# Performance work log

Measured on AMD Instinct MI355X. Metric: run time of the kernel, lower is better.

## Reference

```python
import jax, jax.numpy as jnp
import numpy as np
from jax import lax

LOOKBACK = 336
N_FEATURES = 164
HORIZON = 96
D_MODEL = 64
D_STATE = 16
D_CONV = 4
EXPAND = 2
D_INNER = EXPAND * D_MODEL  # 128
DT_RANK = (D_MODEL + 15) // 16  # 4
MLP_HIDDEN = 64
BATCH = 512


def setup_inputs() -> dict:
    key = jax.random.key(0)
    ks = jax.random.split(key, 20)
    f32 = jnp.float32
    inp = {}
    inp["x_raw"] = jax.random.normal(ks[0], (BATCH, LOOKBACK), f32)
    inp["x_features"] = jax.random.normal(ks[1], (BATCH, N_FEATURES), f32)
    # embed Linear(1, d_model)
    inp["embed_W"] = jax.random.normal(ks[2], (1, D_MODEL), f32) * 0.5
    inp["embed_b"] = jnp.zeros((D_MODEL,), f32)
    # Mamba params (mamba-ssm layout, stored as [in, out] for matmul)
    inp["in_W"] = jax.random.normal(ks[3], (D_MODEL, 2 * D_INNER), f32) * (1.0 / np.sqrt(D_MODEL))
    inp["conv_W"] = jax.random.normal(ks[4], (D_INNER, D_CONV), f32) * 0.3
    inp["conv_b"] = jnp.zeros((D_INNER,), f32)
    inp["xproj_W"] = jax.random.normal(ks[5], (D_INNER, DT_RANK + 2 * D_STATE), f32) * (1.0 / np.sqrt(D_INNER))
    inp["dt_W"] = jax.random.normal(ks[6], (DT_RANK, D_INNER), f32) * (1.0 / np.sqrt(DT_RANK))
    inp["dt_b"] = jax.random.uniform(ks[7], (D_INNER,), f32, -4.0, -2.0)  # softplus -> small dt
    # A_log init = log(arange(1..d_state)) broadcast over d_inner, as in mamba-ssm
    inp["A_log"] = jnp.log(jnp.broadcast_to(jnp.arange(1, D_STATE + 1, dtype=f32), (D_INNER, D_STATE)))
    inp["D"] = jnp.ones((D_INNER,), f32)
    inp["out_W"] = jax.random.normal(ks[8], (D_INNER, D_MODEL), f32) * (1.0 / np.sqrt(D_INNER))
    # MLP stream
    inp["mlp_W1"] = jax.random.normal(ks[9], (N_FEATURES, MLP_HIDDEN), f32) * (1.0 / np.sqrt(N_FEATURES))
    inp["mlp_b1"] = jnp.zeros((MLP_HIDDEN,), f32)
    inp["mlp_W2"] = jax.random.normal(ks[10], (MLP_HIDDEN, MLP_HIDDEN // 2), f32) * (1.0 / np.sqrt(MLP_HIDDEN))
    inp["mlp_b2"] = jnp.zeros((MLP_HIDDEN // 2,), f32)
    # prediction head
    fin = D_MODEL + MLP_HIDDEN // 2
    inp["head_W"] = jax.random.normal(ks[11], (fin, HORIZON), f32) * (1.0 / np.sqrt(fin))
    inp["head_b"] = jnp.zeros((HORIZON,), f32)
    return inp


def silu(x):
    return x * jax.nn.sigmoid(x)


def mamba_block(u, in_W, conv_W, conv_b, xproj_W, dt_W, dt_b, A_log, D, out_W):
    # u: [B, L, d_model]
    B_, L, _ = u.shape
    xz = u @ in_W                      # [B, L, 2*D_INNER]
    x, z = jnp.split(xz, 2, axis=-1)   # each [B, L, D_INNER]
    # causal depthwise conv1d (pad left d_conv-1), then SiLU
    xc = x.transpose(0, 2, 1)          # [B, D_INNER, L]
    kern = conv_W[:, None, :]          # [D_INNER, 1, K] (OIH)
    xc = lax.conv_general_dilated(xc, kern, window_strides=(1,),
                                  padding=[(D_CONV - 1, 0)],
                                  dimension_numbers=("NCH", "OIH", "NCH"),
                                  feature_group_count=D_INNER)
    xc = silu(xc + conv_b[None, :, None])
    x = xc.transpose(0, 2, 1)          # [B, L, D_INNER]
    # input-dependent SSM params
    x_dbl = x @ xproj_W                # [B, L, DT_RANK + 2*D_STATE]
    dt = x_dbl[..., :DT_RANK]
    Bm = x_dbl[..., DT_RANK:DT_RANK + D_STATE]          # [B, L, N]
    Cm = x_dbl[..., DT_RANK + D_STATE:]                 # [B, L, N]
    delta = jax.nn.softplus(dt @ dt_W + dt_b)           # [B, L, D_INNER]
    A = -jnp.exp(A_log)                                 # [D_INNER, N]

    # selective scan over time
    def step(h, inps):
        d_t, B_t, C_t, x_t = inps  # [B,Di], [B,N], [B,N], [B,Di]
        dA = jnp.exp(d_t[:, :, None] * A[None])              # [B, Di, N]
        dBx = (d_t * x_t)[:, :, None] * B_t[:, None, :]      # [B, Di, N]
        h = dA * h + dBx
        y_t = jnp.einsum("bdn,bn->bd", h, C_t)
        return h, y_t

    h0 = jnp.zeros((B_, D_INNER, D_STATE), u.dtype)
    seq = (delta.transpose(1, 0, 2), Bm.transpose(1, 0, 2),
           Cm.transpose(1, 0, 2), x.transpose(1, 0, 2))
    _, ys = lax.scan(step, h0, seq)        # ys: [L, B, D_INNER]
    y = ys.transpose(1, 0, 2) + x * D[None, None, :]
    y = y * silu(z)
    return y @ out_W                        # [B, L, d_model]


def reference(x_raw, x_features, embed_W, embed_b, in_W, conv_W, conv_b,
              xproj_W, dt_W, dt_b, A_log, D, out_W,
              mlp_W1, mlp_b1, mlp_W2, mlp_b2, head_W, head_b):
    # embed raw series: [B, L] -> [B, L, 1] -> [B, L, d_model]
    h = x_raw[..., None] @ embed_W + embed_b
    h = mamba_block(h, in_W, conv_W, conv_b, xproj_W, dt_W, dt_b, A_log, D, out_W)
    h_mamba_out = h[:, -1, :]                       # [B, d_model]
    h_mlp = jax.nn.relu(x_features @ mlp_W1 + mlp_b1) @ mlp_W2 + mlp_b2
    h_final = jnp.concatenate([h_mamba_out, h_mlp], axis=1)
    return h_final @ head_W + head_b                # [B, horizon]
```

## Files before the change

### kernel.cpp

```cpp
#include <hip/hip_runtime.h>
#include <math.h>

#define LOOKBACK 336
#define NFEAT    164
#define HORIZON  96
#define DMODEL   64
#define DSTATE   16
#define DINNER   128
#define MLPH     64
#define BATCH    512
#define XCP      132
#define NG       4
#define GSEG     84
#define CHK      12
#define NCH      7
#define HSTR     20

typedef float v2f __attribute__((ext_vector_type(2)));

__device__ __forceinline__ float fast_rcp(float x) { return __builtin_amdgcn_rcpf(x); }
__device__ __forceinline__ float silu_f(float x) {
    return x * fast_rcp(1.f + __expf(-x));
}

__global__ __launch_bounds__(512, 2) void mamba_one(
    const float* __restrict__ x_raw,   const float* __restrict__ x_features,
    const float* __restrict__ embed_W, const float* __restrict__ embed_b,
    const float* __restrict__ in_W,
    const float* __restrict__ conv_W,  const float* __restrict__ conv_b,
    const float* __restrict__ xproj_W, const float* __restrict__ dt_W,
    const float* __restrict__ dt_b,    const float* __restrict__ A_log,
    const float* __restrict__ Dvec,    const float* __restrict__ out_W,
    const float* __restrict__ mlp_W1,  const float* __restrict__ mlp_b1,
    const float* __restrict__ mlp_W2,  const float* __restrict__ mlp_b2,
    const float* __restrict__ head_W,  const float* __restrict__ head_b,
    float* __restrict__ out)
{
    __shared__ __align__(16) float xrl[344];
    __shared__ __align__(16) float xprojT[20*XCP];
    __shared__ __align__(16) float xcbuf[2][NG][CHK*XCP];
    __shared__ __align__(16) float Bsh[NG][CHK][DSTATE];
    __shared__ __align__(16) float dtraw[NG][CHK][4];
    __shared__ float xcl[DINNER], zsil[DINNER], Cl[DSTATE], yv[DINNER];
    __shared__ float hfin[96], mlph[MLPH];

    const int tid = threadIdx.x;
    const int b   = blockIdx.x;
    const int g   = tid >> 7;
    const int ch  = tid & 127;

    for (int i = tid; i < 339; i += 512)
        xrl[i] = (i >= 3) ? x_raw[b*LOOKBACK + i - 3] : 0.f;
    for (int idx = tid; idx < 20*DINNER; idx += 512) {
        int jj = idx >> 7, d = idx & 127;
        xprojT[jj*XCP + d] = xproj_W[d*36 + jj];
    }

    float w1 = 0.f, w0 = 0.f;
    for (int dm = 0; dm < DMODEL; ++dm) {
        float w = in_W[dm*(2*DINNER) + ch];
        w1 = fmaf(embed_W[dm], w, w1);
        w0 = fmaf(embed_b[dm], w, w0);
    }
    const float4 cw = *(const float4*)&conv_W[ch*4];
    const float  cb = conv_b[ch];
    const float dtw0 = dt_W[ch],       dtw1 = dt_W[128 + ch],
                dtw2 = dt_W[256 + ch], dtw3 = dt_W[384 + ch];
    const float dtb_r = dt_b[ch];
    bool structured = true;
    #pragma unroll
    for (int i = 0; i < 16; ++i) {
        float a = __expf(A_log[ch*DSTATE + i]);
        float ex = (float)(i + 1);
        structured = structured && (fabsf(a - ex) < 1e-3f * ex);
    }
    const bool sfast = __all(structured);
    __syncthreads();

    {
        float* xw = &xcbuf[0][g][0];
        const float* xr = &xrl[g*GSEG];
        if (g == 0) {
            for (int tt = 0; tt < CHK; ++tt) {
                float acc = cb;
                if (tt >= 3) acc = fmaf(fmaf(xr[tt],   w1, w0), cw.x, acc);
                if (tt >= 2) acc = fmaf(fmaf(xr[tt+1], w1, w0), cw.y, acc);
                if (tt >= 1) acc = fmaf(fmaf(xr[tt+2], w1, w0), cw.z, acc);
                acc = fmaf(fmaf(xr[tt+3], w1, w0), cw.w, acc);
                xw[tt*XCP + ch] = silu_f(acc);
            }
        } else {
            float e0 = fmaf(xr[0], w1, w0);
            float e1 = fmaf(xr[1], w1, w0);
            float e2 = fmaf(xr[2], w1, w0);
            #pragma unroll
            for (int tt = 0; tt < CHK; ++tt) {
                float e3 = fmaf(xr[tt+3], w1, w0);
                float acc = cb + e0*cw.x + e1*cw.y + e2*cw.z + e3*cw.w;
                xw[tt*XCP + ch] = silu_f(acc);
                e0 = e1; e1 = e2; e2 = e3;
            }
        }
    }
    __syncthreads();

    v2f h01={0,0},h23={0,0},h45={0,0},h67={0,0},
        h89={0,0},hAB={0,0},hCD={0,0},hEF={0,0};
    float dacc = 0.f;

    for (int c = 0; c < NCH; ++c) {
        const int buf = c & 1;

        if (ch < 120) {
            const int tt = ch / 10;
            const int j0 = (ch - tt*10) * 2;
            const float* p0   = &xprojT[j0*XCP];
            const float* p1   = &xprojT[(j0+1)*XCP];
            const float* xrow = &xcbuf[buf][g][tt*XCP];
            v2f a0 = {0,0}, a1 = {0,0};
            #pragma unroll 8
            for (int d = 0; d < DINNER; d += 4) {
                float4 xv = *(const float4*)(xrow + d);
                float4 q0 = *(const float4*)(p0 + d);
                float4 q1 = *(const float4*)(p1 + d);
                v2f xl = {xv.x, xv.y}, xh = {xv.z, xv.w};
                v2f q0l = {q0.x, q0.y}, q0h = {q0.z, q0.w};
                v2f q1l = {q1.x, q1.y}, q1h = {q1.z, q1.w};
                a0 = __builtin_elementwise_fma(xl, q0l, a0);
                a0 = __builtin_elementwise_fma(xh, q0h, a0);
                a1 = __builtin_elementwise_fma(xl, q1l, a1);
                a1 = __builtin_elementwise_fma(xh, q1h, a1);
            }
            float r0 = a0.x + a0.y, r1 = a1.x + a1.y;
            if (j0 < 4) *(float2*)&dtraw[g][tt][j0] = make_float2(r0, r1);
            else        *(float2*)&Bsh[g][tt][j0-4] = make_float2(r0, r1);
        }
        __syncthreads();

        const float* xs = &xcbuf[buf][g][0];
        if (__builtin_expect(sfast, 1)) {
            #pragma unroll
            for (int tt = 0; tt < CHK; ++tt) {
                float4 dr = *(const float4*)&dtraw[g][tt][0];
                float dv = fmaf(dr.x, dtw0, fmaf(dr.y, dtw1,
                           fmaf(dr.z, dtw2, fmaf(dr.w, dtw3, dtb_r))));
                float e  = __expf(dv);
                float p  = 1.f + e;
                float r  = fast_rcp(p);
                float dl = (dv > 80.f) ? dv : __logf(p);
                dacc += dl;
                float ux = dl * xs[tt*XCP + ch];
                float4 B0 = *(const float4*)&Bsh[g][tt][0];
                float4 B1 = *(const float4*)&Bsh[g][tt][4];
                float4 B2 = *(const float4*)&Bsh[g][tt][8];
                float4 B3 = *(const float4*)&Bsh[g][tt][12];
                float r2 = r*r;
                v2f r2v = {r2, r2};
                v2f p01 = {r, r2};
                v2f p23 = p01*r2v, p45 = p23*r2v, p67 = p45*r2v, p89 = p67*r2v,
                    pAB = p89*r2v, pCD = pAB*r2v, pEF = pCD*r2v;
                v2f uxv = {ux, ux};
                h01 = __builtin_elementwise_fma(p01, h01, uxv*(v2f){B0.x,B0.y});
                h23 = __builtin_elementwise_fma(p23, h23, uxv*(v2f){B0.z,B0.w});
                h45 = __builtin_elementwise_fma(p45, h45, uxv*(v2f){B1.x,B1.y});
                h67 = __builtin_elementwise_fma(p67, h67, uxv*(v2f){B1.z,B1.w});
                h89 = __builtin_elementwise_fma(p89, h89, uxv*(v2f){B2.x,B2.y});
                hAB = __builtin_elementwise_fma(pAB, hAB, uxv*(v2f){B2.z,B2.w});
                hCD = __builtin_elementwise_fma(pCD, hCD, uxv*(v2f){B3.x,B3.y});
                hEF = __builtin_elementwise_fma(pEF, hEF, uxv*(v2f){B3.z,B3.w});
            }
        } else {
            const float* Arow = A_log + ch*DSTATE;
            for (int tt = 0; tt < CHK; ++tt) {
                float4 dr = *(const float4*)&dtraw[g][tt][0];
                float dv = fmaf(dr.x, dtw0, fmaf(dr.y, dtw1,
                           fmaf(dr.z, dtw2, fmaf(dr.w, dtw3, dtb_r))));
                float e  = __expf(dv);
                float dl = (dv > 15.f) ? dv : __logf(1.f + e);
                dacc += dl;
                float ux = dl * xs[tt*XCP + ch];
                const float* Brow = &Bsh[g][tt][0];
                float hv[16] = {h01.x,h01.y,h23.x,h23.y,h45.x,h45.y,h67.x,h67.y,
                                h89.x,h89.y,hAB.x,hAB.y,hCD.x,hCD.y,hEF.x,hEF.y};
                for (int i = 0; i < 16; ++i)
                    hv[i] = fmaf(__expf(-__expf(Arow[i])*dl), hv[i], ux*Brow[i]);
                h01=(v2f){hv[0],hv[1]};   h23=(v2f){hv[2],hv[3]};
                h45=(v2f){hv[4],hv[5]};   h67=(v2f){hv[6],hv[7]};
                h89=(v2f){hv[8],hv[9]};   hAB=(v2f){hv[10],hv[11]};
                hCD=(v2f){hv[12],hv[13]}; hEF=(v2f){hv[14],hv[15]};
            }
        }

        if (c + 1 < NCH) {
            float* xw = &xcbuf[buf^1][g][0];
            const float* xr = &xrl[g*GSEG + (c+1)*CHK];
            float e0 = fmaf(xr[0], w1, w0);
            float e1 = fmaf(xr[1], w1, w0);
            float e2 = fmaf(xr[2], w1, w0);
            float v = 0.f;
            #pragma unroll
            for (int tt = 0; tt < CHK; ++tt) {
                float e3 = fmaf(xr[tt+3], w1, w0);
                float acc = cb + e0*cw.x + e1*cw.y + e2*cw.z + e3*cw.w;
                v = silu_f(acc);
                xw[tt*XCP + ch] = v;
                e0 = e1; e1 = e2; e2 = e3;
            }
            if (g == NG-1 && c + 1 == NCH-1) xcl[ch] = v;
        }
        __syncthreads();
    }

    float* hpart = &xcbuf[0][0][0];
    float* dsum  = &Bsh[0][0][0];
    {
        float4* hp = (float4*)&hpart[(g*128 + ch)*HSTR];
        hp[0] = make_float4(h01.x,h01.y,h23.x,h23.y);
        hp[1] = make_float4(h45.x,h45.y,h67.x,h67.y);
        hp[2] = make_float4(h89.x,h89.y,hAB.x,hAB.y);
        hp[3] = make_float4(hCD.x,hCD.y,hEF.x,hEF.y);
        dsum[g*128 + ch] = dacc;
    }
    __syncthreads();

    float H[16];
    if (tid < 128) {
        {
            const float4* hp = (const float4*)&hpart[tid*HSTR];
            float4 a = hp[0], bq = hp[1], cq = hp[2], dq = hp[3];
            H[0]=a.x;  H[1]=a.y;  H[2]=a.z;  H[3]=a.w;
            H[4]=bq.x; H[5]=bq.y; H[6]=bq.z; H[7]=bq.w;
            H[8]=cq.x; H[9]=cq.y; H[10]=cq.z;H[11]=cq.w;
            H[12]=dq.x;H[13]=dq.y;H[14]=dq.z;H[15]=dq.w;
        }
        for (int gg = 1; gg < NG; ++gg) {
            float D = dsum[gg*128 + tid];
            const float4* hp = (const float4*)&hpart[(gg*128 + tid)*HSTR];
            float4 a = hp[0], bq = hp[1], cq = hp[2], dq = hp[3];
            float hg[16] = {a.x,a.y,a.z,a.w,bq.x,bq.y,bq.z,bq.w,
                            cq.x,cq.y,cq.z,cq.w,dq.x,dq.y,dq.z,dq.w};
            if (structured) {
                float r = __expf(-D);
                float pw = 1.f;
                #pragma unroll
                for (int i = 0; i < 16; ++i) {
                    pw *= r;
                    H[i] = fmaf(pw, H[i], hg[i]);
                }
            } else {
                #pragma unroll
                for (int i = 0; i < 16; ++i)
                    H[i] = fmaf(__expf(-__expf(A_log[tid*DSTATE+i])*D), H[i], hg[i]);
            }
        }
    } else if (tid < 256) {
        const int c2 = tid - 128;
        float a1 = 0.f, a0 = 0.f;
        for (int dm = 0; dm < DMODEL; ++dm) {
            float w = in_W[dm*(2*DINNER) + DINNER + c2];
            a1 = fmaf(embed_W[dm], w, a1);
            a0 = fmaf(embed_b[dm], w, a0);
        }
        float zv = fmaf(xrl[338], a1, a0);
        zsil[c2] = silu_f(zv);
    } else if (tid < 320) {
        const int lane = tid - 256;
        const int n = lane & 15, q = lane >> 4;
        float acc = 0.f;
        for (int d = q*32; d < q*32 + 32; ++d)
            acc = fmaf(xcl[d], xproj_W[d*36 + 20 + n], acc);
        acc += __shfl_xor(acc, 16);
        acc += __shfl_xor(acc, 32);
        if (lane < 16) Cl[n] = acc;
    } else if (tid >= 384) {
        const int lane = tid - 384;
        const int j = lane >> 1, k = lane & 1;
        const float* xf = x_features + b*NFEAT;
        float acc = 0.f;
        const int f0 = k*82, f1 = (k ? NFEAT : 82);
        for (int f = f0; f < f1; ++f)
            acc = fmaf(xf[f], mlp_W1[f*MLPH + j], acc);
        acc += __shfl_xor(acc, 1);
        if (k == 0) mlph[j] = fmaxf(acc + mlp_b1[j], 0.f);
    }
    __syncthreads();

    if (tid < 128) {
        float acc = 0.f;
        #pragma unroll
        for (int i = 0; i < 16; ++i) acc = fmaf(H[i], Cl[i], acc);
        float y = acc + xcl[tid]*Dvec[tid];
        yv[tid] = y * zsil[tid];
    } else if (tid < 192) {
        const int lane = tid - 128;
        const int j = lane >> 1, k = lane & 1;
        float acc = 0.f;
        for (int kk = k*32; kk < k*32 + 32; ++kk)
            acc = fmaf(mlph[kk], mlp_W2[kk*32 + j], acc);
        acc += __shfl_xor(acc, 1);
        if (k == 0) hfin[64 + j] = acc + mlp_b2[j];
    }
    __syncthreads();

    if (tid < 256) {
        const int o = tid >> 2, k = tid & 3;
        float acc = 0.f;
        for (int d = k*32; d < k*32 + 32; ++d)
            acc = fmaf(yv[d], out_W[d*DMODEL + o], acc);
        acc += __shfl_xor(acc, 1);
        acc += __shfl_xor(acc, 2);
        if (k == 0) hfin[o] = acc;
    }
    __syncthreads();

    if (tid < 192) {
        const int o = tid >> 1, k = tid & 1;
        float acc = 0.f;
        for (int i = k*48; i < k*48 + 48; ++i)
            acc = fmaf(hfin[i], head_W[i*HORIZON + o], acc);
        acc += __shfl_xor(acc, 1);
        if (k == 0) out[b*HORIZON + o] = acc + head_b[o];
    }
}

extern "C" void kernel_launch(void* const* d_in, const int* in_sizes, int n_in,
                              void* d_out, int out_size, void* d_ws, size_t ws_size,
                              hipStream_t stream) {
    (void)in_sizes; (void)n_in; (void)out_size; (void)d_ws; (void)ws_size;
    mamba_one<<<BATCH, 512, 0, stream>>>(
        (const float*)d_in[0],  (const float*)d_in[1],  (const float*)d_in[2],
        (const float*)d_in[3],  (const float*)d_in[4],  (const float*)d_in[5],
        (const float*)d_in[6],  (const float*)d_in[7],  (const float*)d_in[8],
        (const float*)d_in[9],  (const float*)d_in[10], (const float*)d_in[11],
        (const float*)d_in[12], (const float*)d_in[13], (const float*)d_in[14],
        (const float*)d_in[15], (const float*)d_in[16], (const float*)d_in[17],
        (const float*)d_in[18], (float*)d_out);
}
```

Baseline: 173.2 us.

## Split sequence scan into eight segments with 1024-thread blocks and tree merge

Doubles the number of time segments scanned in parallel per batch element, going from 4 to 8 groups of 128 channels with 1024 threads per block and half-length chunks. The x_proj work is remapped across 480 threads so each chunk's dt/B projection covers all groups, and the shared buffer gets padded group strides. The final state combine becomes a three-level pairwise tree merge in shared memory instead of a serial loop over segments. This shortens the sequential recurrence per thread but adds more barriers and merge steps, and the larger block may lower occupancy and raise register pressure.

New measurement: 215.0 us. 1.24x slower.

```diff
diff --git a/kernel.cpp b/kernel.cpp
--- a/kernel.cpp
+++ b/kernel.cpp
@@ -10,10 +10,11 @@
 #define MLPH     64
 #define BATCH    512
 #define XCP      132
-#define NG       4
-#define GSEG     84
-#define CHK      12
+#define NG       8
+#define GSEG     42
+#define CHK      6
 #define NCH      7
+#define GST      (CHK*XCP + 4)
 #define HSTR     20
 
 typedef float v2f __attribute__((ext_vector_type(2)));
@@ -23,7 +24,7 @@
     return x * fast_rcp(1.f + __expf(-x));
 }
 
-__global__ __launch_bounds__(512, 2) void mamba_one(
+__global__ __launch_bounds__(1024, 2) void mamba_one(
     const float* __restrict__ x_raw,   const float* __restrict__ x_features,
     const float* __restrict__ embed_W, const float* __restrict__ embed_b,
     const float* __restrict__ in_W,
@@ -38,7 +39,7 @@
 {
     __shared__ __align__(16) float xrl[344];
     __shared__ __align__(16) float xprojT[20*XCP];
-    __shared__ __align__(16) float xcbuf[2][NG][CHK*XCP];
+    __shared__ __align__(16) float xcbuf[2][NG*GST];
     __shared__ __align__(16) float Bsh[NG][CHK][DSTATE];
     __shared__ __align__(16) float dtraw[NG][CHK][4];
     __shared__ float xcl[DINNER], zsil[DINNER], Cl[DSTATE], yv[DINNER];
@@ -49,9 +50,9 @@
     const int g   = tid >> 7;
     const int ch  = tid & 127;
 
-    for (int i = tid; i < 339; i += 512)
+    for (int i = tid; i < 339; i += 1024)
         xrl[i] = (i >= 3) ? x_raw[b*LOOKBACK + i - 3] : 0.f;
-    for (int idx = tid; idx < 20*DINNER; idx += 512) {
+    for (int idx = tid; idx < 20*DINNER; idx += 1024) {
         int jj = idx >> 7, d = idx & 127;
         xprojT[jj*XCP + d] = xproj_W[d*36 + jj];
     }
@@ -75,10 +76,15 @@
         structured = structured && (fabsf(a - ex) < 1e-3f * ex);
     }
     const bool sfast = __all(structured);
+
+    const int a2jp  = tid / 48;
+    const int a2rem = tid - a2jp*48;
+    const int a2tt  = a2rem >> 3;
+    const int a2g   = a2rem & 7;
     __syncthreads();
 
     {
-        float* xw = &xcbuf[0][g][0];
+        float* xw = &xcbuf[0][g*GST];
         const float* xr = &xrl[g*GSEG];
         if (g == 0) {
             for (int tt = 0; tt < CHK; ++tt) {
@@ -111,12 +117,11 @@
     for (int c = 0; c < NCH; ++c) {
         const int buf = c & 1;
 
-        if (ch < 120) {
-            const int tt = ch / 10;
-            const int j0 = (ch - tt*10) * 2;
+        if (tid < 480) {
+            const int j0 = a2jp*2;
             const float* p0   = &xprojT[j0*XCP];
             const float* p1   = &xprojT[(j0+1)*XCP];
-            const float* xrow = &xcbuf[buf][g][tt*XCP];
+            const float* xrow = &xcbuf[buf][a2g*GST + a2tt*XCP];
             v2f a0 = {0,0}, a1 = {0,0};
             #pragma unroll 8
             for (int d = 0; d < DINNER; d += 4) {
@@ -132,12 +137,12 @@
                 a1 = __builtin_elementwise_fma(xh, q1h, a1);
             }
             float r0 = a0.x + a0.y, r1 = a1.x + a1.y;
-            if (j0 < 4) *(float2*)&dtraw[g][tt][j0] = make_float2(r0, r1);
-            else        *(float2*)&Bsh[g][tt][j0-4] = make_float2(r0, r1);
+            if (j0 < 4) *(float2*)&dtraw[a2g][a2tt][j0] = make_float2(r0, r1);
+            else        *(float2*)&Bsh[a2g][a2tt][j0-4] = make_float2(r0, r1);
         }
         __syncthreads();
 
-        const float* xs = &xcbuf[buf][g][0];
+        const float* xs = &xcbuf[buf][g*GST];
         if (__builtin_expect(sfast, 1)) {
             #pragma unroll
             for (int tt = 0; tt < CHK; ++tt) {
@@ -192,7 +197,7 @@
         }
 
         if (c + 1 < NCH) {
-            float* xw = &xcbuf[buf^1][g][0];
+            float* xw = &xcbuf[buf^1][g*GST];
             const float* xr = &xrl[g*GSEG + (c+1)*CHK];
             float e0 = fmaf(xr[0], w1, w0);
             float e1 = fmaf(xr[1], w1, w0);
@@ -211,60 +216,56 @@
         __syncthreads();
     }
 
-    float* hpart = &xcbuf[0][0][0];
-    float* dsum  = &Bsh[0][0][0];
-    {
-        float4* hp = (float4*)&hpart[(g*128 + ch)*HSTR];
-        hp[0] = make_float4(h01.x,h01.y,h23.x,h23.y);
-        hp[1] = make_float4(h45.x,h45.y,h67.x,h67.y);
-        hp[2] = make_float4(h89.x,h89.y,hAB.x,hAB.y);
-        hp[3] = make_float4(hCD.x,hCD.y,hEF.x,hEF.y);
-        dsum[g*128 + ch] = dacc;
-    }
-    __syncthreads();
-
-    float H[16];
-    if (tid < 128) {
-        {
-            const float4* hp = (const float4*)&hpart[tid*HSTR];
-            float4 a = hp[0], bq = hp[1], cq = hp[2], dq = hp[3];
-            H[0]=a.x;  H[1]=a.y;  H[2]=a.z;  H[3]=a.w;
-            H[4]=bq.x; H[5]=bq.y; H[6]=bq.z; H[7]=bq.w;
-            H[8]=cq.x; H[9]=cq.y; H[10]=cq.z;H[11]=cq.w;
-            H[12]=dq.x;H[13]=dq.y;H[14]=dq.z;H[15]=dq.w;
-        }
-        for (int gg = 1; gg < NG; ++gg) {
-            float D = dsum[gg*128 + tid];
-            const float4* hp = (const float4*)&hpart[(gg*128 + tid)*HSTR];
-            float4 a = hp[0], bq = hp[1], cq = hp[2], dq = hp[3];
-            float hg[16] = {a.x,a.y,a.z,a.w,bq.x,bq.y,bq.z,bq.w,
-                            cq.x,cq.y,cq.z,cq.w,dq.x,dq.y,dq.z,dq.w};
-            if (structured) {
-                float r = __expf(-D);
-                float pw = 1.f;
-                #pragma unroll
-                for (int i = 0; i < 16; ++i) {
-                    pw *= r;
-                    H[i] = fmaf(pw, H[i], hg[i]);
-                }
-            } else {
-                #pragma unroll
-                for (int i = 0; i < 16; ++i)
-                    H[i] = fmaf(__expf(-__expf(A_log[tid*DSTATE+i])*D), H[i], hg[i]);
-            }
-        }
-    } else if (tid < 256) {
-        const int c2 = tid - 128;
+    float* hpart = &xcbuf[0][0];
+
+    auto writeRec = [&](int rec) {
+        float* p = &hpart[rec*HSTR];
+        *(float4*)(p+0)  = make_float4(h01.x,h01.y,h23.x,h23.y);
+        *(float4*)(p+4)  = make_float4(h45.x,h45.y,h67.x,h67.y);
+        *(float4*)(p+8)  = make_float4(h89.x,h89.y,hAB.x,hAB.y);
+        *(float4*)(p+12) = make_float4(hCD.x,hCD.y,hEF.x,hEF.y);
+        p[16] = dacc;
+    };
+    auto mergeRec = [&](int rec) {
+        const float* p = &hpart[rec*HSTR];
+        float4 a  = *(const float4*)(p+0),  bq = *(const float4*)(p+4);
+        float4 cq = *(const float4*)(p+8),  dq = *(const float4*)(p+12);
+        float Ld = p[16];
+        float hg[16] = {a.x,a.y,a.z,a.w,bq.x,bq.y,bq.z,bq.w,
+                        cq.x,cq.y,cq.z,cq.w,dq.x,dq.y,dq.z,dq.w};
+        float hv[16] = {h01.x,h01.y,h23.x,h23.y,h45.x,h45.y,h67.x,h67.y,
+                        h89.x,h89.y,hAB.x,hAB.y,hCD.x,hCD.y,hEF.x,hEF.y};
+        if (structured) {
+            float r = __expf(-Ld);
+            float pw = 1.f;
+            #pragma unroll
+            for (int i = 0; i < 16; ++i) { pw *= r; hv[i] = fmaf(pw, hv[i], hg[i]); }
+        } else {
+            #pragma unroll
+            for (int i = 0; i < 16; ++i)
+                hv[i] = fmaf(__expf(-__expf(A_log[ch*DSTATE+i])*Ld), hv[i], hg[i]);
+        }
+        dacc += Ld;
+        h01=(v2f){hv[0],hv[1]};   h23=(v2f){hv[2],hv[3]};
+        h45=(v2f){hv[4],hv[5]};   h67=(v2f){hv[6],hv[7]};
+        h89=(v2f){hv[8],hv[9]};   hAB=(v2f){hv[10],hv[11]};
+        hCD=(v2f){hv[12],hv[13]}; hEF=(v2f){hv[14],hv[15]};
+    };
+
+    if (g & 1) writeRec((g >> 1)*128 + ch);
+    __syncthreads();
+    if (!(g & 1)) {
+        mergeRec((g >> 1)*128 + ch);
+    } else if (g == 1) {
         float a1 = 0.f, a0 = 0.f;
         for (int dm = 0; dm < DMODEL; ++dm) {
-            float w = in_W[dm*(2*DINNER) + DINNER + c2];
+            float w = in_W[dm*(2*DINNER) + DINNER + ch];
             a1 = fmaf(embed_W[dm], w, a1);
             a0 = fmaf(embed_b[dm], w, a0);
         }
-        float zv = fmaf(xrl[338], a1, a0);
-        zsil[c2] = silu_f(zv);
-    } else if (tid < 320) {
-        const int lane = tid - 256;
+        zsil[ch] = silu_f(fmaf(xrl[338], a1, a0));
+    } else if (tid >= 384 && tid < 448) {
+        const int lane = tid - 384;
         const int n = lane & 15, q = lane >> 4;
         float acc = 0.f;
         for (int d = q*32; d < q*32 + 32; ++d)
@@ -272,8 +273,8 @@
         acc += __shfl_xor(acc, 16);
         acc += __shfl_xor(acc, 32);
         if (lane < 16) Cl[n] = acc;
-    } else if (tid >= 384) {
-        const int lane = tid - 384;
+    } else if (g == 7) {
+        const int lane = tid - 896;
         const int j = lane >> 1, k = lane & 1;
         const float* xf = x_features + b*NFEAT;
         float acc = 0.f;
@@ -285,10 +286,21 @@
     }
     __syncthreads();
 
+    if (g == 2 || g == 6) writeRec(((g >> 2) << 7) + ch);
+    __syncthreads();
+    if (g == 0 || g == 4) mergeRec(((g >> 2) << 7) + ch);
+    __syncthreads();
+
+    if (g == 4) writeRec(ch);
+    __syncthreads();
+    if (g == 0) mergeRec(ch);
+    __syncthreads();
+
     if (tid < 128) {
-        float acc = 0.f;
-        #pragma unroll
-        for (int i = 0; i < 16; ++i) acc = fmaf(H[i], Cl[i], acc);
+        float acc = h01.x*Cl[0] + h01.y*Cl[1] + h23.x*Cl[2] + h23.y*Cl[3]
+                  + h45.x*Cl[4] + h45.y*Cl[5] + h67.x*Cl[6] + h67.y*Cl[7]
+                  + h89.x*Cl[8] + h89.y*Cl[9] + hAB.x*Cl[10] + hAB.y*Cl[11]
+                  + hCD.x*Cl[12] + hCD.y*Cl[13] + hEF.x*Cl[14] + hEF.y*Cl[15];
         float y = acc + xcl[tid]*Dvec[tid];
         yv[tid] = y * zsil[tid];
     } else if (tid < 192) {
@@ -327,7 +339,7 @@
                               void* d_out, int out_size, void* d_ws, size_t ws_size,
                               hipStream_t stream) {
     (void)in_sizes; (void)n_in; (void)out_size; (void)d_ws; (void)ws_size;
-    mamba_one<<<BATCH, 512, 0, stream>>>(
+    mamba_one<<<BATCH, 1024, 0, stream>>>(
         (const float*)d_in[0],  (const float*)d_in[1],  (const float*)d_in[2],
         (const float*)d_in[3],  (const float*)d_in[4],  (const float*)d_in[5],
         (const float*)d_in[6],  (const float*)d_in[7],  (const float*)d_in[8],
```
